# Kernel tuning notes

Hardware: AMD Instinct MI355X
Metric: run time of the kernel (lower is better)

Reference implementation:

```python
import jax, jax.numpy as jnp
import numpy as np

N_HEADS = 8
D_K = 64
SCALE = D_K ** -0.5


def setup_inputs() -> dict:
    key = jax.random.key(0)
    k1, k2, k3, k4, k5 = jax.random.split(key, 5)
    C = 512
    inner = N_HEADS * D_K  # 512
    return {
        "x": jax.random.normal(k1, (16, C, 32, 32), dtype=jnp.float32),
        "W_qkv": jax.random.normal(k2, (C, 3 * inner), dtype=jnp.float32) * (C ** -0.5),
        "b_qkv": jax.random.normal(k3, (3 * inner,), dtype=jnp.float32) * 0.02,
        "W_out": jax.random.normal(k4, (inner, C), dtype=jnp.float32) * (inner ** -0.5),
        "b_out": jax.random.normal(k5, (C,), dtype=jnp.float32) * 0.02,
    }


def reference(x, W_qkv, b_qkv, W_out, b_out):
    B, C, H, W = x.shape
    N = H * W
    xt = x.reshape(B, C, N).transpose(0, 2, 1)  # (B, N, C) tokens
    qkv = (xt @ W_qkv + b_qkv).reshape(B, N, N_HEADS, 3 * D_K)
    q, k, v = jnp.split(qkv, 3, axis=-1)  # each (B, N, H, d_k)
    # scores over key axis j; softmax along j (original dim=2 of bijh)
    attn = jnp.einsum('bihd,bjhd->bhij', q, k) * SCALE
    attn = jax.nn.softmax(attn, axis=-1)
    res = jnp.einsum('bhij,bjhd->bihd', attn, v).reshape(B, N, N_HEADS * D_K)
    res = res @ W_out + b_out + xt  # out projection + residual (note: GroupNorm unused in source forward)
    return res.transpose(0, 2, 1).reshape(B, C, H, W)
```

## Files before the change

### kernel.cpp

```cpp
#include <hip/hip_runtime.h>
#include <hip/hip_bf16.h>
#include <stdint.h>

#define N_HEADS 8
#define D_K 64
#define QSCALE (0.125f * 1.44269504088896f)

typedef __attribute__((ext_vector_type(4))) float f32x4;
typedef __attribute__((ext_vector_type(16))) float f32x16;
typedef __attribute__((ext_vector_type(8))) short bf16x8;
typedef __attribute__((ext_vector_type(4))) unsigned short u16x4;
typedef __attribute__((ext_vector_type(4))) unsigned int u32x4;

#define AS1 __attribute__((address_space(1)))
#define AS3 __attribute__((address_space(3)))

static __device__ __forceinline__ void gload_lds16(const void* g, void* l) {
    __builtin_amdgcn_global_load_lds((const AS1 void*)g, (AS3 void*)l, 16, 0, 0);
}

static __device__ __forceinline__ __hip_bfloat16 f2bf(float f) {
    return __float2bfloat16(f);
}

static __device__ __forceinline__ unsigned short bfbits(float f) {
    return __builtin_bit_cast(unsigned short, __float2bfloat16(f));
}

static __device__ __forceinline__ uint32_t pkbf(float lo, float hi) {
    return (uint32_t)bfbits(lo) | ((uint32_t)bfbits(hi) << 16);
}

static __device__ __forceinline__ float fexp2(float x) {
#if __has_builtin(__builtin_amdgcn_exp2f)
    return __builtin_amdgcn_exp2f(x);
#else
    float r;
    asm("v_exp_f32 %0, %1" : "=v"(r) : "v"(x));
    return r;
#endif
}

static __device__ __forceinline__ float fmax3(float a, float b, float c) {
    return fmaxf(fmaxf(a, b), c);
}

__global__ void transpose_bf16(const float* __restrict__ in,
                               __hip_bfloat16* __restrict__ out,
                               int R, int C) {
    __shared__ float tile[32][33];
    const int bz = blockIdx.z;
    const int r0 = blockIdx.y * 32, c0 = blockIdx.x * 32;
    const float* ip = in + (size_t)bz * R * C;
    __hip_bfloat16* op = out + (size_t)bz * R * C;
    const int tx = threadIdx.x, ty = threadIdx.y;
#pragma unroll
    for (int i = 0; i < 4; ++i)
        tile[ty + i * 8][tx] = ip[(size_t)(r0 + ty + i * 8) * C + c0 + tx];
    __syncthreads();
#pragma unroll
    for (int i = 0; i < 4; ++i)
        op[(size_t)(c0 + ty + i * 8) * R + r0 + tx] = f2bf(tile[tx][ty + i * 8]);
}

__device__ __forceinline__ void gemm128_tile(
    const __hip_bfloat16* __restrict__ Abase, int lda,
    const __hip_bfloat16* __restrict__ Bbase, int ldb,
    int K,
    __hip_bfloat16* Atile, __hip_bfloat16* Btile,
    f32x4 (&acc)[4][4]) {
    const int t = threadIdx.x;
    const int w = t >> 6;
    const int l = t & 63;
    const int wr = (w >> 1) * 64, wc = (w & 1) * 64;
    const int fr = l & 15, fq = l >> 4;

#pragma unroll
    for (int m = 0; m < 4; ++m)
#pragma unroll
        for (int n = 0; n < 4; ++n) acc[m][n] = (f32x4)0.f;

    auto stage = [&](int buf, int k0) {
#pragma unroll
        for (int i = 0; i < 2; ++i) {
            const int tt = t + i * 256;
            const int row = tt >> 2;
            const int sl = (tt & 3) ^ (row & 3);
            char* la = (char*)Atile + buf * 8192 + i * 4096 + w * 1024;
            char* lb = (char*)Btile + buf * 8192 + i * 4096 + w * 1024;
            gload_lds16(Abase + (size_t)row * lda + k0 + sl * 8, la);
            gload_lds16(Bbase + (size_t)row * ldb + k0 + sl * 8, lb);
        }
    };

    const int nkt = K >> 5;
    stage(0, 0);
    __syncthreads();

    for (int kt = 0; kt < nkt; ++kt) {
        const int cur = kt & 1;
        if (kt + 1 < nkt) stage(cur ^ 1, (kt + 1) * 32);

        const char* Ab = (const char*)Atile + cur * 8192;
        const char* Bb = (const char*)Btile + cur * 8192;
        bf16x8 af[4], bfr[4];
#pragma unroll
        for (int m = 0; m < 4; ++m) {
            const int row = wr + m * 16 + fr;
            af[m] = *(const bf16x8*)(Ab + ((row * 64 + fq * 16) ^ ((row & 3) << 4)));
        }
#pragma unroll
        for (int n = 0; n < 4; ++n) {
            const int row = wc + n * 16 + fr;
            bfr[n] = *(const bf16x8*)(Bb + ((row * 64 + fq * 16) ^ ((row & 3) << 4)));
        }
#pragma unroll
        for (int m = 0; m < 4; ++m)
#pragma unroll
            for (int n = 0; n < 4; ++n)
                acc[m][n] = __builtin_amdgcn_mfma_f32_16x16x32_bf16(af[m], bfr[n], acc[m][n], 0, 0, 0);

        __syncthreads();
    }
}

__global__ __launch_bounds__(256) void qkv_gemm(
    const __hip_bfloat16* __restrict__ xt,
    const __hip_bfloat16* __restrict__ Wqt,
    const float* __restrict__ bias,
    __hip_bfloat16* __restrict__ q_ws,
    __hip_bfloat16* __restrict__ k_ws,
    __hip_bfloat16* __restrict__ v_ws) {
    __shared__ __attribute__((aligned(16))) __hip_bfloat16 Atile[2][128 * 32];
    __shared__ __attribute__((aligned(16))) __hip_bfloat16 Btile[2][128 * 32];
    const int id0 = blockIdx.x;
    const int wg = (id0 & 7) * 192 + (id0 >> 3);
    const int tn = wg % 12;
    const int tm = (wg / 12) & 7;
    const int b  = wg / 96;
    f32x4 acc[4][4];
    gemm128_tile(xt + ((size_t)b * 1024 + tm * 128) * 512, 512,
                 Wqt + (size_t)tn * 128 * 512, 512, 512,
                 &Atile[0][0], &Btile[0][0], acc);

    const int t = threadIdx.x, l = t & 63, w = t >> 6;
    const int wr = (w >> 1) * 64, wc = (w & 1) * 64, fr = l & 15, fq = l >> 4;
#pragma unroll
    for (int m = 0; m < 4; ++m) {
#pragma unroll
        for (int n = 0; n < 4; ++n) {
            const int j = tn * 128 + wc + n * 16 + fr;
            const int h = j / 192, rem = j % 192, p = rem / 64, d = rem % 64;
            const float bj = bias[j];
            const size_t bh = (size_t)b * 8 + h;
#pragma unroll
            for (int r = 0; r < 4; ++r) {
                const int nn = tm * 128 + wr + m * 16 + fq * 4 + r;
                const float v = acc[m][n][r] + bj;
                if (p == 0)      q_ws[(bh * 1024 + nn) * 64 + d] = f2bf(v * QSCALE);
                else if (p == 1) k_ws[(bh * 1024 + nn) * 64 + d] = f2bf(v);
                else             v_ws[(bh * 64 + d) * 1024 + nn] = f2bf(v);
            }
        }
    }
}

__global__ __launch_bounds__(256) void attn_kernel(
    const __hip_bfloat16* __restrict__ q_ws,
    const __hip_bfloat16* __restrict__ k_ws,
    const __hip_bfloat16* __restrict__ v_ws,
    __hip_bfloat16* __restrict__ ao) {
    __shared__ __attribute__((aligned(16))) __hip_bfloat16 KtS[2][64 * 64];
    __shared__ __attribute__((aligned(16))) __hip_bfloat16 VtS[2][64 * 64];

    const int id = blockIdx.x;
    const int bh = id & 127;
    const int qt = id >> 7;
    const int t = threadIdx.x, l = t & 63, w = t >> 6;
    const int lq = l & 31, hi = l >> 5;
    const int qrow = qt * 128 + w * 32 + lq;
    const int swz = (lq & 7) << 4;

    const __hip_bfloat16* qp = q_ws + ((size_t)bh * 1024 + qrow) * 64;
    bf16x8 qb[4];
#pragma unroll
    for (int s = 0; s < 4; ++s) qb[s] = *(const bf16x8*)(qp + s * 16 + hi * 8);

    f32x16 oacc[2];
    oacc[0] = (f32x16)0.f; oacc[1] = (f32x16)0.f;
    float m = -1e30f, lsum = 0.f;

    const __hip_bfloat16* kbase = k_ws + (size_t)bh * 1024 * 64;
    const __hip_bfloat16* vbase = v_ws + (size_t)bh * 64 * 1024;

    auto stage = [&](int buf, int kt2) {
#pragma unroll
        for (int i = 0; i < 2; ++i) {
            const int tt = t + i * 256;
            const int row = tt >> 3;
            const int sl = (tt & 7) ^ (row & 7);
            char* kd = (char*)&KtS[buf][0] + w * 1024 + i * 4096;
            char* vd = (char*)&VtS[buf][0] + w * 1024 + i * 4096;
            gload_lds16(kbase + (size_t)(kt2 * 64 + row) * 64 + sl * 8, kd);
            gload_lds16(vbase + (size_t)row * 1024 + kt2 * 64 + sl * 8, vd);
        }
    };

    stage(0, 0);
    __syncthreads();

    for (int kt = 0; kt < 16; ++kt) {
        const int cur = kt & 1;
        if (kt < 15) stage(cur ^ 1, kt + 1);

        const char* KtC = (const char*)&KtS[cur][0];
        const char* VtC = (const char*)&VtS[cur][0];

        f32x16 s0 = (f32x16)0.f, s1 = (f32x16)0.f;
        __builtin_amdgcn_s_setprio(1);
#pragma unroll
        for (int s = 0; s < 4; ++s) {
            const int colb = s * 32 + hi * 16;
            bf16x8 k0 = *(const bf16x8*)(KtC + ((lq * 128 + colb) ^ swz));
            bf16x8 k1 = *(const bf16x8*)(KtC + (((32 + lq) * 128 + colb) ^ swz));
            s0 = __builtin_amdgcn_mfma_f32_32x32x16_bf16(k0, qb[s], s0, 0, 0, 0);
            s1 = __builtin_amdgcn_mfma_f32_32x32x16_bf16(k1, qb[s], s1, 0, 0, 0);
        }
        __builtin_amdgcn_s_setprio(0);

        float c0 = fmax3(s0[0], s0[1], s0[2]);
        float c1 = fmax3(s0[4], s0[5], s0[6]);
        float c2 = fmax3(s0[8], s0[9], s0[10]);
        float c3 = fmax3(s0[12], s0[13], s0[14]);
        c0 = fmax3(c0, s0[3], s1[0]);
        c1 = fmax3(c1, s0[7], s1[4]);
        c2 = fmax3(c2, s0[11], s1[8]);
        c3 = fmax3(c3, s0[15], s1[12]);
        c0 = fmax3(c0, s1[1], s1[2]);
        c1 = fmax3(c1, s1[5], s1[6]);
        c2 = fmax3(c2, s1[9], s1[10]);
        c3 = fmax3(c3, s1[13], s1[14]);
        c0 = fmax3(c0, s1[3], c1);
        c2 = fmax3(c2, s1[7], s1[11]);
        float pmax = fmax3(c0, c2, fmaxf(c3, s1[15]));
        pmax = fmaxf(pmax, __shfl_xor(pmax, 32, 64));

        if (__any(pmax - m > 8.f)) {
            const float mn = fmaxf(m, pmax);
            const float corr = fexp2(m - mn);
            m = mn;
            lsum *= corr;
#pragma unroll
            for (int i = 0; i < 16; ++i) { oacc[0][i] *= corr; oacc[1][i] *= corr; }
        }

        float la0 = 0.f, la1 = 0.f, la2 = 0.f, la3 = 0.f;
#pragma unroll
        for (int i = 0; i < 16; i += 4) {
            s0[i + 0] = fexp2(s0[i + 0] - m); la0 += s0[i + 0];
            s0[i + 1] = fexp2(s0[i + 1] - m); la1 += s0[i + 1];
            s0[i + 2] = fexp2(s0[i + 2] - m); la2 += s0[i + 2];
            s0[i + 3] = fexp2(s0[i + 3] - m); la3 += s0[i + 3];
        }
#pragma unroll
        for (int i = 0; i < 16; i += 4) {
            s1[i + 0] = fexp2(s1[i + 0] - m); la0 += s1[i + 0];
            s1[i + 1] = fexp2(s1[i + 1] - m); la1 += s1[i + 1];
            s1[i + 2] = fexp2(s1[i + 2] - m); la2 += s1[i + 2];
            s1[i + 3] = fexp2(s1[i + 3] - m); la3 += s1[i + 3];
        }
        lsum += (la0 + la1) + (la2 + la3);

#pragma unroll
        for (int s = 0; s < 4; ++s) {
            const int rb = (s & 1) * 8;
            uint32_t pk01, pk23, pk45, pk67;
            if (s < 2) {
                pk01 = pkbf(s0[rb + 0], s0[rb + 1]); pk23 = pkbf(s0[rb + 2], s0[rb + 3]);
                pk45 = pkbf(s0[rb + 4], s0[rb + 5]); pk67 = pkbf(s0[rb + 6], s0[rb + 7]);
            } else {
                pk01 = pkbf(s1[rb + 0], s1[rb + 1]); pk23 = pkbf(s1[rb + 2], s1[rb + 3]);
                pk45 = pkbf(s1[rb + 4], s1[rb + 5]); pk67 = pkbf(s1[rb + 6], s1[rb + 7]);
            }
            const uint32_t sentA = hi ? pk01 : pk45;
            const uint32_t sentB = hi ? pk23 : pk67;
            const uint32_t recvA = (uint32_t)__shfl_xor((int)sentA, 32, 64);
            const uint32_t recvB = (uint32_t)__shfl_xor((int)sentB, 32, 64);
            u32x4 fw;
            fw[0] = hi ? recvA : pk01;
            fw[1] = hi ? recvB : pk23;
            fw[2] = hi ? pk45 : recvA;
            fw[3] = hi ? pk67 : recvB;
            const bf16x8 pf = __builtin_bit_cast(bf16x8, fw);

            const int colb = s * 32 + hi * 16;
            bf16x8 v0 = *(const bf16x8*)(VtC + ((lq * 128 + colb) ^ swz));
            bf16x8 v1 = *(const bf16x8*)(VtC + (((32 + lq) * 128 + colb) ^ swz));
            __builtin_amdgcn_s_setprio(1);
            oacc[0] = __builtin_amdgcn_mfma_f32_32x32x16_bf16(v0, pf, oacc[0], 0, 0, 0);
            oacc[1] = __builtin_amdgcn_mfma_f32_32x32x16_bf16(v1, pf, oacc[1], 0, 0, 0);
            __builtin_amdgcn_s_setprio(0);
        }

        __syncthreads();
    }

    lsum += __shfl_xor(lsum, 32, 64);
    const float inv = 1.f / lsum;
    const int b = bh >> 3, h = bh & 7;
    __hip_bfloat16* aop = ao + ((size_t)b * 1024 + qrow) * 512 + h * 64;
#pragma unroll
    for (int dd = 0; dd < 2; ++dd)
#pragma unroll
        for (int rg = 0; rg < 4; ++rg) {
            u16x4 pkd;
#pragma unroll
            for (int j = 0; j < 4; ++j)
                pkd[j] = bfbits(oacc[dd][rg * 4 + j] * inv);
            const int d0 = dd * 32 + rg * 8 + hi * 4;
            *(u16x4*)(aop + d0) = pkd;
        }
}

__global__ __launch_bounds__(256) void out_gemm(
    const __hip_bfloat16* __restrict__ Wot,
    const __hip_bfloat16* __restrict__ ao,
    const float* __restrict__ bias,
    const float* __restrict__ x,
    float* __restrict__ out) {
    __shared__ __attribute__((aligned(16))) __hip_bfloat16 Atile[2][128 * 32];
    __shared__ __attribute__((aligned(16))) __hip_bfloat16 Btile[2][128 * 32];
    const int id0 = blockIdx.x;
    const int wg = (id0 & 7) * 64 + (id0 >> 3);
    const int tn = wg & 7;
    const int tc = (wg >> 3) & 3;
    const int b  = wg >> 5;
    f32x4 acc[4][4];
    gemm128_tile(Wot + (size_t)tc * 128 * 512, 512,
                 ao + ((size_t)b * 1024 + tn * 128) * 512, 512, 512,
                 &Atile[0][0], &Btile[0][0], acc);

    const int t = threadIdx.x, l = t & 63, w = t >> 6;
    const int wr = (w >> 1) * 64, wc = (w & 1) * 64, fr = l & 15, fq = l >> 4;
#pragma unroll
    for (int m = 0; m < 4; ++m) {
#pragma unroll
        for (int n = 0; n < 4; ++n) {
            const int nn = tn * 128 + wc + n * 16 + fr;
#pragma unroll
            for (int r = 0; r < 4; ++r) {
                const int c = tc * 128 + wr + m * 16 + fq * 4 + r;
                const size_t idx = ((size_t)b * 512 + c) * 1024 + nn;
                out[idx] = acc[m][n][r] + bias[c] + x[idx];
            }
        }
    }
}

extern "C" void kernel_launch(void* const* d_in, const int* in_sizes, int n_in,
                              void* d_out, int out_size, void* d_ws, size_t ws_size,
                              hipStream_t stream) {
    const float* x     = (const float*)d_in[0];
    const float* W_qkv = (const float*)d_in[1];
    const float* b_qkv = (const float*)d_in[2];
    const float* W_out = (const float*)d_in[3];
    const float* b_out = (const float*)d_in[4];
    float* out = (float*)d_out;

    const int B = 16, C = 512, N = 1024, BH = B * N_HEADS;

    char* ws = (char*)d_ws;
    __hip_bfloat16* xt   = (__hip_bfloat16*)ws; ws += (size_t)B * N * C * 2;
    __hip_bfloat16* Wqt  = (__hip_bfloat16*)ws; ws += (size_t)1536 * 512 * 2;
    __hip_bfloat16* Wot  = (__hip_bfloat16*)ws; ws += (size_t)512 * 512 * 2;
    __hip_bfloat16* q_ws = (__hip_bfloat16*)ws; ws += (size_t)BH * N * 64 * 2;
    __hip_bfloat16* k_ws = (__hip_bfloat16*)ws; ws += (size_t)BH * N * 64 * 2;
    __hip_bfloat16* v_ws = (__hip_bfloat16*)ws; ws += (size_t)BH * 64 * N * 2;
    __hip_bfloat16* ao   = (__hip_bfloat16*)ws; ws += (size_t)B * N * 512 * 2;

    transpose_bf16<<<dim3(N / 32, C / 32, B), dim3(32, 8), 0, stream>>>(x, xt, C, N);
    transpose_bf16<<<dim3(1536 / 32, 512 / 32, 1), dim3(32, 8), 0, stream>>>(W_qkv, Wqt, 512, 1536);
    transpose_bf16<<<dim3(512 / 32, 512 / 32, 1), dim3(32, 8), 0, stream>>>(W_out, Wot, 512, 512);

    qkv_gemm<<<dim3(1536), 256, 0, stream>>>(xt, Wqt, b_qkv, q_ws, k_ws, v_ws);

    attn_kernel<<<dim3(1024), 256, 0, stream>>>(q_ws, k_ws, v_ws, ao);

    out_gemm<<<dim3(512), 256, 0, stream>>>(Wot, ao, b_out, x, out);
}
```

Before: 155.9 us.

## Store K/V in MFMA-fragment order and load V directly from global

The QKV projection epilogue now writes K and V into a pre-tiled layout that matches the per-lane MFMA operand order, so each lane's 16-byte fragment is contiguous. The attention kernel stages K into LDS with plain linear copies and no swizzle, and drops the V LDS buffer entirely, reading V fragments straight from global memory after the score MFMAs. This cuts LDS traffic and footprint and removes the address swizzle math. In exchange, the V reads go to global/L2 with latency that may not be hidden, and the scattered K stores in the epilogue may be less coalesced.

```diff
diff --git a/kernel.cpp b/kernel.cpp
--- a/kernel.cpp
+++ b/kernel.cpp
@@ -147,19 +147,35 @@
     const int wr = (w >> 1) * 64, wc = (w & 1) * 64, fr = l & 15, fq = l >> 4;
 #pragma unroll
     for (int m = 0; m < 4; ++m) {
+        const int nnb = tm * 128 + wr + m * 16 + fq * 4;
 #pragma unroll
         for (int n = 0; n < 4; ++n) {
             const int j = tn * 128 + wc + n * 16 + fr;
             const int h = j / 192, rem = j % 192, p = rem / 64, d = rem % 64;
             const float bj = bias[j];
             const size_t bh = (size_t)b * 8 + h;
-#pragma unroll
-            for (int r = 0; r < 4; ++r) {
-                const int nn = tm * 128 + wr + m * 16 + fq * 4 + r;
-                const float v = acc[m][n][r] + bj;
-                if (p == 0)      q_ws[(bh * 1024 + nn) * 64 + d] = f2bf(v * QSCALE);
-                else if (p == 1) k_ws[(bh * 1024 + nn) * 64 + d] = f2bf(v);
-                else             v_ws[(bh * 64 + d) * 1024 + nn] = f2bf(v);
+            float vv[4];
+#pragma unroll
+            for (int r = 0; r < 4; ++r) vv[r] = acc[m][n][r] + bj;
+            if (p == 0) {
+#pragma unroll
+                for (int r = 0; r < 4; ++r)
+                    q_ws[(bh * 1024 + nnb + r) * 64 + d] = f2bf(vv[r] * QSCALE);
+            } else if (p == 1) {
+                const int base = (nnb >> 6) * 4096 + (d >> 4) * 1024 +
+                                 ((nnb >> 5) & 1) * 512 + ((d >> 3) & 1) * 256 +
+                                 (nnb & 31) * 8 + (d & 7);
+                __hip_bfloat16* kp = k_ws + bh * 65536 + base;
+#pragma unroll
+                for (int r = 0; r < 4; ++r) kp[r * 8] = f2bf(vv[r]);
+            } else {
+                const int base = (nnb >> 6) * 4096 + ((nnb >> 4) & 3) * 1024 +
+                                 (d >> 5) * 512 +
+                                 (((nnb >> 3) & 1) * 32 + (d & 31)) * 8 + (nnb & 7);
+                u16x4 pk;
+#pragma unroll
+                for (int r = 0; r < 4; ++r) pk[r] = bfbits(vv[r]);
+                *(u16x4*)(v_ws + bh * 65536 + base) = pk;
             }
         }
     }
@@ -170,8 +186,7 @@
     const __hip_bfloat16* __restrict__ k_ws,
     const __hip_bfloat16* __restrict__ v_ws,
     __hip_bfloat16* __restrict__ ao) {
-    __shared__ __attribute__((aligned(16))) __hip_bfloat16 KtS[2][64 * 64];
-    __shared__ __attribute__((aligned(16))) __hip_bfloat16 VtS[2][64 * 64];
+    __shared__ __attribute__((aligned(16))) __hip_bfloat16 KtS[2][4096];
 
     const int id = blockIdx.x;
     const int bh = id & 127;
@@ -179,7 +194,6 @@
     const int t = threadIdx.x, l = t & 63, w = t >> 6;
     const int lq = l & 31, hi = l >> 5;
     const int qrow = qt * 128 + w * 32 + lq;
-    const int swz = (lq & 7) << 4;
 
     const __hip_bfloat16* qp = q_ws + ((size_t)bh * 1024 + qrow) * 64;
     bf16x8 qb[4];
@@ -190,19 +204,15 @@
     oacc[0] = (f32x16)0.f; oacc[1] = (f32x16)0.f;
     float m = -1e30f, lsum = 0.f;
 
-    const __hip_bfloat16* kbase = k_ws + (size_t)bh * 1024 * 64;
-    const __hip_bfloat16* vbase = v_ws + (size_t)bh * 64 * 1024;
+    const __hip_bfloat16* kbase = k_ws + (size_t)bh * 65536;
+    const char* vbase = (const char*)(v_ws + (size_t)bh * 65536);
 
     auto stage = [&](int buf, int kt2) {
 #pragma unroll
         for (int i = 0; i < 2; ++i) {
             const int tt = t + i * 256;
-            const int row = tt >> 3;
-            const int sl = (tt & 7) ^ (row & 7);
             char* kd = (char*)&KtS[buf][0] + w * 1024 + i * 4096;
-            char* vd = (char*)&VtS[buf][0] + w * 1024 + i * 4096;
-            gload_lds16(kbase + (size_t)(kt2 * 64 + row) * 64 + sl * 8, kd);
-            gload_lds16(vbase + (size_t)row * 1024 + kt2 * 64 + sl * 8, vd);
+            gload_lds16(kbase + (size_t)kt2 * 4096 + tt * 8, kd);
         }
     };
 
@@ -214,19 +224,25 @@
         if (kt < 15) stage(cur ^ 1, kt + 1);
 
         const char* KtC = (const char*)&KtS[cur][0];
-        const char* VtC = (const char*)&VtS[cur][0];
 
         f32x16 s0 = (f32x16)0.f, s1 = (f32x16)0.f;
         __builtin_amdgcn_s_setprio(1);
 #pragma unroll
         for (int s = 0; s < 4; ++s) {
-            const int colb = s * 32 + hi * 16;
-            bf16x8 k0 = *(const bf16x8*)(KtC + ((lq * 128 + colb) ^ swz));
-            bf16x8 k1 = *(const bf16x8*)(KtC + (((32 + lq) * 128 + colb) ^ swz));
+            bf16x8 k0 = *(const bf16x8*)(KtC + s * 2048 + l * 16);
+            bf16x8 k1 = *(const bf16x8*)(KtC + s * 2048 + 1024 + l * 16);
             s0 = __builtin_amdgcn_mfma_f32_32x32x16_bf16(k0, qb[s], s0, 0, 0, 0);
             s1 = __builtin_amdgcn_mfma_f32_32x32x16_bf16(k1, qb[s], s1, 0, 0, 0);
         }
         __builtin_amdgcn_s_setprio(0);
+
+        const char* vpc = vbase + (size_t)kt * 8192;
+        bf16x8 vf0[4], vf1[4];
+#pragma unroll
+        for (int s = 0; s < 4; ++s) {
+            vf0[s] = *(const bf16x8*)(vpc + s * 2048 + l * 16);
+            vf1[s] = *(const bf16x8*)(vpc + s * 2048 + 1024 + l * 16);
+        }
 
         float c0 = fmax3(s0[0], s0[1], s0[2]);
         float c1 = fmax3(s0[4], s0[5], s0[6]);
@@ -293,12 +309,9 @@
             fw[3] = hi ? pk67 : recvB;
             const bf16x8 pf = __builtin_bit_cast(bf16x8, fw);
 
-            const int colb = s * 32 + hi * 16;
-            bf16x8 v0 = *(const bf16x8*)(VtC + ((lq * 128 + colb) ^ swz));
-            bf16x8 v1 = *(const bf16x8*)(VtC + (((32 + lq) * 128 + colb) ^ swz));
             __builtin_amdgcn_s_setprio(1);
-            oacc[0] = __builtin_amdgcn_mfma_f32_32x32x16_bf16(v0, pf, oacc[0], 0, 0, 0);
-            oacc[1] = __builtin_amdgcn_mfma_f32_32x32x16_bf16(v1, pf, oacc[1], 0, 0, 0);
+            oacc[0] = __builtin_amdgcn_mfma_f32_32x32x16_bf16(vf0[s], pf, oacc[0], 0, 0, 0);
+            oacc[1] = __builtin_amdgcn_mfma_f32_32x32x16_bf16(vf1[s], pf, oacc[1], 0, 0, 0);
             __builtin_amdgcn_s_setprio(0);
         }
 
```

Result: faster. 142.5 us (-8.6%).
